# Optimization experiments

Measured on AMD Instinct MI355X. Metric: run time of the kernel, lower is better.

The kernel has to match this reference:

```python
import jax, jax.numpy as jnp
import numpy as np

B, H1, W1 = 2, 64, 64
H2, W2 = 64, 64
DIM = 64    # query_latent_dim
CLD = 128   # cost_latent_dim
K = 8       # latent tokens in cost memory
HEADS = 8
CH = 1      # cost_heads_num
R = 4


def layer_norm(x, g, b, eps=1e-5):
    m = x.mean(-1, keepdims=True)
    v = ((x - m) ** 2).mean(-1, keepdims=True)
    return (x - m) / jnp.sqrt(v + eps) * g + b


def lin_pos_emb(x, dim):
    # LinearPositionEmbeddingSine: x [N,1,2] -> [N,1,dim]
    freq = jnp.linspace(0.0, dim // 4 - 1, dim // 4)
    a = 3.14 * x[..., 0:1] * freq / 200.0
    b = 3.14 * x[..., 1:2] * freq / 200.0
    return jnp.concatenate([jnp.sin(a), jnp.cos(a), jnp.sin(b), jnp.cos(b)], axis=-1)


def bilinear_sample(img, coords):
    # img: [N,C,H,W]; coords: [N,h,w,2] (x,y) pixel coords; zero padding, align_corners=True
    N, C, H, W = img.shape
    x, y = coords[..., 0], coords[..., 1]
    x0 = jnp.floor(x); y0 = jnp.floor(y)
    wx = x - x0; wy = y - y0
    nidx = jnp.arange(N)[:, None, None]

    def gather(xi, yi):
        valid = ((xi >= 0) & (xi <= W - 1) & (yi >= 0) & (yi <= H - 1)).astype(img.dtype)
        xc = jnp.clip(xi, 0, W - 1).astype(jnp.int32)
        yc = jnp.clip(yi, 0, H - 1).astype(jnp.int32)
        return img[nidx, :, yc, xc] * valid[..., None]  # [N,h,w,C]

    v00 = gather(x0, y0); v10 = gather(x0 + 1.0, y0)
    v01 = gather(x0, y0 + 1.0); v11 = gather(x0 + 1.0, y0 + 1.0)
    out = (v00 * ((1 - wx) * (1 - wy))[..., None] + v10 * (wx * (1 - wy))[..., None]
           + v01 * ((1 - wx) * wy)[..., None] + v11 * (wx * wy)[..., None])
    return out.transpose(0, 3, 1, 2)  # [N,C,h,w]


def encode_flow(cost_maps, coords1):
    b, _, h1, w1 = coords1.shape
    c = coords1.transpose(0, 2, 3, 1)  # [B,H1,W1,2]
    d = jnp.linspace(-float(R), float(R), 2 * R + 1)
    dy, dx = jnp.meshgrid(d, d, indexing='ij')
    delta = jnp.stack([dy, dx], axis=-1)  # [9,9,2]
    centroid = c.reshape(b * h1 * w1, 1, 1, 2)
    samp = centroid + delta[None]  # [B*H1*W1,9,9,2]
    corr = bilinear_sample(cost_maps, samp)  # [B*H1*W1,CH,9,9]
    return corr.reshape(b, h1, w1, -1).transpose(0, 3, 1, 2)  # [B,81*CH,H1,W1]


def upsample_flow(flow, mask):
    # convex upsample [H,W] -> [8H,8W]
    n, _, h, w = flow.shape
    m = jax.nn.softmax(mask.reshape(n, 1, 9, 8, 8, h, w), axis=2)
    f = jnp.pad(8.0 * flow, ((0, 0), (0, 0), (1, 1), (1, 1)))
    patches = jnp.stack([f[:, :, i:i + h, j:j + w] for i in range(3) for j in range(3)], axis=2)
    up = jnp.sum(m * patches[:, :, :, None, None], axis=2)  # [N,2,8,8,H,W]
    return up.transpose(0, 1, 4, 2, 5, 3).reshape(n, 2, 8 * h, 8 * w)


def setup_inputs() -> dict:
    key = jax.random.key(0)
    ks = jax.random.split(key, 16)
    Bn = B * H1 * W1
    ys, xs = np.meshgrid(np.arange(H1), np.arange(W1), indexing='ij')
    grid = jnp.asarray(np.stack([xs, ys], 0), jnp.float32)  # [2,H1,W1], (x,y)
    coords1 = jnp.broadcast_to(grid, (B, 2, H1, W1)) + 3.0 * jax.random.normal(ks[0], (B, 2, H1, W1), jnp.float32)
    s = 0.05
    return {
        'cost_maps': jax.random.normal(ks[1], (Bn, CH, H2, W2), jnp.float32),
        'cost_memory': jax.random.normal(ks[2], (Bn, K, CLD), jnp.float32),
        'coords1': coords1,
        'up_mask': jax.random.normal(ks[3], (B, 9 * 64, H1, W1), jnp.float32),
        'fte_w1': s * jax.random.normal(ks[4], (DIM, 81 * CH), jnp.float32),
        'fte_b1': jnp.zeros((DIM,), jnp.float32),
        'fte_w2': s * jax.random.normal(ks[5], (DIM, DIM), jnp.float32),
        'fte_b2': jnp.zeros((DIM,), jnp.float32),
        'ln1_g': jnp.ones((DIM,), jnp.float32),
        'ln1_b': jnp.zeros((DIM,), jnp.float32),
        'ln2_g': jnp.ones((DIM,), jnp.float32),
        'ln2_b': jnp.zeros((DIM,), jnp.float32),
        'wq': s * jax.random.normal(ks[6], (DIM, DIM), jnp.float32),
        'bq': jnp.zeros((DIM,), jnp.float32),
        'wk': s * jax.random.normal(ks[7], (CLD, DIM), jnp.float32),
        'bk': jnp.zeros((DIM,), jnp.float32),
        'wv': s * jax.random.normal(ks[8], (CLD, DIM), jnp.float32),
        'bv': jnp.zeros((DIM,), jnp.float32),
        'wp': s * jax.random.normal(ks[9], (2 * DIM, DIM), jnp.float32),
        'bp': jnp.zeros((DIM,), jnp.float32),
        'ffn_w1': s * jax.random.normal(ks[10], (DIM, DIM), jnp.float32),
        'ffn_b1': jnp.zeros((DIM,), jnp.float32),
        'ffn_w2': s * jax.random.normal(ks[11], (DIM, DIM), jnp.float32),
        'ffn_b2': jnp.zeros((DIM,), jnp.float32),
    }


def reference(cost_maps, cost_memory, coords1, up_mask,
              fte_w1, fte_b1, fte_w2, fte_b2,
              ln1_g, ln1_b, ln2_g, ln2_b,
              wq, bq, wk, bk, wv, bv, wp, bp,
              ffn_w1, ffn_b1, ffn_w2, ffn_b2):
    Bn = B * H1 * W1
    ys, xs = jnp.meshgrid(jnp.arange(H1, dtype=coords1.dtype), jnp.arange(W1, dtype=coords1.dtype), indexing='ij')
    coords0 = jnp.broadcast_to(jnp.stack([xs, ys], 0), (B, 2, H1, W1))

    # correlation-volume bilinear sampling (encode_flow_token)
    corr = encode_flow(cost_maps, coords1)  # [B,81*CH,H1,W1]

    # flow token encoder: 1x1 conv -> GELU -> 1x1 conv
    q = jnp.einsum('bchw,oc->bohw', corr, fte_w1) + fte_b1[None, :, None, None]
    q = jax.nn.gelu(q, approximate=False)
    q = jnp.einsum('bchw,oc->bohw', q, fte_w2) + fte_b2[None, :, None, None]
    query = q.transpose(0, 2, 3, 1).reshape(Bn, 1, DIM)

    # cross attention with linear sine position encoding of query coords
    qc = coords1.reshape(B, 2, H1 * W1).transpose(0, 2, 1).reshape(Bn, 1, 2)
    enc = lin_pos_emb(qc, DIM)
    short = query
    qn = layer_norm(query, ln1_g, ln1_b)
    qlin = (qn + enc) @ wq + bq            # [Bn,1,DIM]
    k = cost_memory @ wk + bk              # [Bn,K,DIM]
    v = cost_memory @ wv + bv
    hd = DIM // HEADS
    qh = qlin.reshape(Bn, 1, HEADS, hd).transpose(0, 2, 1, 3)
    kh = k.reshape(Bn, K, HEADS, hd).transpose(0, 2, 1, 3)
    vh = v.reshape(Bn, K, HEADS, hd).transpose(0, 2, 1, 3)
    attn = jax.nn.softmax(jnp.einsum('bhid,bhjd->bhij', qh, kh) * (hd ** -0.5), axis=-1)
    out = jnp.einsum('bhij,bhjd->bhid', attn, vh).transpose(0, 2, 1, 3).reshape(Bn, 1, DIM)
    x = jnp.concatenate([out, short], -1) @ wp + bp
    x = short + x
    xn = layer_norm(x, ln2_g, ln2_b)
    x = x + (jax.nn.gelu(xn @ ffn_w1 + ffn_b1, approximate=False) @ ffn_w2 + ffn_b2)
    cost_global = x.reshape(B, H1, W1, DIM).transpose(0, 3, 1, 2)

    # convex upsampling of the flow field
    flow_up = upsample_flow(coords1 - coords0, up_mask)  # [B,2,8*H1,8*W1]
    return (flow_up, cost_global)
```

## Files before the change

kernel.cpp:

```cpp
#include <hip/hip_runtime.h>
#include <math.h>

typedef _Float16 h2 __attribute__((ext_vector_type(2)));

#if __has_builtin(__builtin_amdgcn_fdot2)
#define FDOT2(a,b,c) __builtin_amdgcn_fdot2((a),(b),(c),false)
#else
__device__ __forceinline__ float FDOT2(h2 a, h2 b, float c){
    return c + (float)a.x*(float)b.x + (float)a.y*(float)b.y;
}
#endif

__device__ __forceinline__ h2 pk2(float x, float y){
#if __has_builtin(__builtin_amdgcn_cvt_pkrtz)
    return __builtin_bit_cast(h2, __builtin_amdgcn_cvt_pkrtz(x, y));
#else
    h2 r; r.x = (_Float16)x; r.y = (_Float16)y; return r;
#endif
}
__device__ __forceinline__ unsigned h2u(h2 v){ return __builtin_bit_cast(unsigned, v); }
__device__ __forceinline__ h2 uh2(unsigned v){ return __builtin_bit_cast(h2, v); }

__device__ __forceinline__ float fast_rcp(float x){
#if __has_builtin(__builtin_amdgcn_rcpf)
    return __builtin_amdgcn_rcpf(x);
#else
    return 1.f/x;
#endif
}

__device__ __forceinline__ float dot8(uint4 w, uint4 v, float acc){
    acc = FDOT2(uh2(w.x), uh2(v.x), acc);
    acc = FDOT2(uh2(w.y), uh2(v.y), acc);
    acc = FDOT2(uh2(w.z), uh2(v.z), acc);
    acc = FDOT2(uh2(w.w), uh2(v.w), acc);
    return acc;
}

__device__ __forceinline__ float gelu_exact(float x){
    return 0.5f * x * (1.0f + erff(x * 0.70710678118654752f));
}

__device__ __forceinline__ void ln_stats(float x, float& mean, float& inv){
    float s1 = x, s2 = x*x;
    #pragma unroll
    for(int off = 32; off >= 1; off >>= 1){
        s1 += __shfl_xor(s1, off, 64);
        s2 += __shfl_xor(s2, off, 64);
    }
    mean = s1 * (1.f/64.f);
    float var = fmaxf(s2 * (1.f/64.f) - mean*mean, 0.f);
    inv = rsqrtf(var + 1e-5f);
}

__device__ __forceinline__ void lds_fence(){ __asm__ volatile("s_waitcnt lgkmcnt(0)" ::: "memory"); }

#define W1T_OFF 0
#define W2T_OFF 2816
#define WQ_OFF  5120
#define FW1_OFF 7424
#define FW2_OFF 9728
#define WV_OFF  12032
#define WP_OFF  16384
#define WK_OFF  20736
#define WTOT    25344

#define CMO   0
#define TUO   544
#define CORRO 544
#define QPO   1088
#define CCO   1124
#define PIXDW 1188
#define NWAVES 12
#define LDSDW (WTOT + NWAVES*PIXDW)

__global__ void prep_weights(const float* __restrict__ w1, const float* __restrict__ w2,
                             const float* __restrict__ wq, const float* __restrict__ fw1,
                             const float* __restrict__ fw2, const float* __restrict__ wv,
                             const float* __restrict__ wp, const float* __restrict__ wk,
                             unsigned* __restrict__ ws){
    int idx = blockIdx.x * blockDim.x + threadIdx.x;
    if(idx >= WTOT) return;
    float a = 0.f, b = 0.f;
    if(idx < W2T_OFF){
        int t = idx / 44, cp = idx % 44;
        if(2*cp   < 81) a = w1[t*81 + 2*cp];
        if(2*cp+1 < 81) b = w1[t*81 + 2*cp+1];
    } else if(idx < WQ_OFF){
        int r = idx - W2T_OFF; int t = r / 36, cp = r % 36;
        if(cp < 32){ a = w2[t*64 + 2*cp]; b = w2[t*64 + 2*cp+1]; }
    } else if(idx < FW1_OFF){
        int r = idx - WQ_OFF; int t = r / 36, cp = r % 36;
        if(cp < 32){ a = wq[(2*cp)*64 + t]; b = wq[(2*cp+1)*64 + t]; }
    } else if(idx < FW2_OFF){
        int r = idx - FW1_OFF; int t = r / 36, cp = r % 36;
        if(cp < 32){ a = fw1[(2*cp)*64 + t]; b = fw1[(2*cp+1)*64 + t]; }
    } else if(idx < WV_OFF){
        int r = idx - FW2_OFF; int t = r / 36, cp = r % 36;
        if(cp < 32){ a = fw2[(2*cp)*64 + t]; b = fw2[(2*cp+1)*64 + t]; }
    } else if(idx < WP_OFF){
        int r = idx - WV_OFF; int t = r / 68, cp = r % 68;
        if(cp < 64){ a = wv[(2*cp)*64 + t]; b = wv[(2*cp+1)*64 + t]; }
    } else if(idx < WK_OFF){
        int r = idx - WP_OFF; int t = r / 68, cp = r % 68;
        if(cp < 64){ a = wp[(2*cp)*64 + t]; b = wp[(2*cp+1)*64 + t]; }
    } else {
        int r = idx - WK_OFF; int c = r / 36, hp = r % 36;
        if(hp < 32){ a = wk[c*64 + 2*hp]; b = wk[c*64 + 2*hp+1]; }
    }
    ws[idx] = h2u(pk2(a, b));
}

__device__ __forceinline__ float bilin(const float* __restrict__ cmap, float cx, float cy, int e){
    int i = e / 9, j = e - 9*i;
    float sx = cx + (float)(i - 4);
    float sy = cy + (float)(j - 4);
    float x0 = floorf(sx), y0 = floorf(sy);
    float wx = sx - x0,   wy = sy - y0;
    float acc = 0.f;
    #pragma unroll
    for(int dy = 0; dy < 2; dy++){
        #pragma unroll
        for(int dx = 0; dx < 2; dx++){
            float xf = x0 + (float)dx, yf = y0 + (float)dy;
            bool valid = (xf >= 0.f) && (xf <= 63.f) && (yf >= 0.f) && (yf <= 63.f);
            int xi = min(max((int)xf, 0), 63);
            int yi = min(max((int)yf, 0), 63);
            float v = valid ? cmap[yi*64 + xi] : 0.f;
            acc += v * ((dx ? wx : 1.f - wx) * (dy ? wy : 1.f - wy));
        }
    }
    return acc;
}

__global__ __launch_bounds__(768, 1) void decoder_main(
    const float* __restrict__ cost_maps, const float* __restrict__ cost_memory,
    const float* __restrict__ coords1, const float* __restrict__ up_mask,
    const unsigned* __restrict__ ws,
    const float* __restrict__ fte_b1, const float* __restrict__ fte_b2,
    const float* __restrict__ ln1_g, const float* __restrict__ ln1_b,
    const float* __restrict__ ln2_g, const float* __restrict__ ln2_b,
    const float* __restrict__ bq, const float* __restrict__ bv,
    const float* __restrict__ bp, const float* __restrict__ fb1,
    const float* __restrict__ fb2, float* __restrict__ out)
{
    __shared__ unsigned sm[LDSDW];

    const int tid = threadIdx.x;
    const int wv  = tid >> 6;
    const int ln  = tid & 63;
    const int gw  = blockIdx.x * NWAVES + wv;
    const int nPix = (gw < 2048) ? 3 : 2;

    int pix = gw;
    const float4* cm4p = (const float4*)cost_memory;
    float4 cmv0 = cm4p[(size_t)pix*256 +   0 + ln];
    float4 cmv1 = cm4p[(size_t)pix*256 +  64 + ln];
    float4 cmv2 = cm4p[(size_t)pix*256 + 128 + ln];
    float4 cmv3 = cm4p[(size_t)pix*256 + 192 + ln];
    float cx = coords1[(pix >> 12)*8192 + (pix & 4095)];
    float cy = coords1[(pix >> 12)*8192 + 4096 + (pix & 4095)];

    {
        const uint4* src = (const uint4*)ws;
        uint4* dst = (uint4*)sm;
        for(int i = tid; i < WTOT/4; i += 768) dst[i] = src[i];
    }
    const float b1v = fte_b1[ln], b2v = fte_b2[ln];
    const float g1v = ln1_g[ln], be1 = ln1_b[ln];
    const float g2v = ln2_g[ln], be2 = ln2_b[ln];
    const float bqv = bq[ln], bvv = bv[ln], bpv = bp[ln];
    const float f1v = fb1[ln], f2v = fb2[ln];
    __syncthreads();

    float* out_cg = out + 2*2*512*512;
    unsigned* P = sm + WTOT + wv * PIXDW;

    const int h_ = ln & 7;
    const int c0 = ln >> 3;
    const int j_ = ln >> 3;
    const int h3 = ln >> 3;

    #pragma unroll 1
    for(int g = 0; g < nPix; g++){
        {
            float4 v; int l0, jt, cp0;
            #define STAGE(V, I4) \
                v = V; l0 = 4*((I4)*64 + ln); jt = l0 >> 7; cp0 = (l0 & 127) >> 1; \
                { uint2 pw; pw.x = h2u(pk2(v.x, v.y)); pw.y = h2u(pk2(v.z, v.w)); \
                  *(uint2*)&P[CMO + jt*68 + cp0] = pw; }
            STAGE(cmv0, 0) STAGE(cmv1, 1) STAGE(cmv2, 2) STAGE(cmv3, 3)
            #undef STAGE
        }
        {
            const float* cmap = cost_maps + (size_t)pix * 4096;
            float cv = bilin(cmap, cx, cy, ln);
            float c2 = bilin(cmap, cx, cy, 64 + ln);
            float pr = __shfl_xor(cv, 1, 64);
            if((ln & 1) == 0) P[CORRO + (ln >> 1)] = h2u(pk2(cv, pr));
            float pr2 = __shfl_xor(c2, 1, 64);
            if(ln < 17 && (ln & 1) == 0){
                float bb = (ln == 16) ? 0.f : pr2;
                P[CORRO + 32 + (ln >> 1)] = h2u(pk2(c2, bb));
            }
            if(ln < 3) P[CORRO + 41 + ln] = 0u;
        }
        int npix = pix + 3072;
        float4 n0, n1, n2, n3; float ncx = 0.f, ncy = 0.f;
        if(g + 1 < nPix){
            n0 = cm4p[(size_t)npix*256 +   0 + ln];
            n1 = cm4p[(size_t)npix*256 +  64 + ln];
            n2 = cm4p[(size_t)npix*256 + 128 + ln];
            n3 = cm4p[(size_t)npix*256 + 192 + ln];
            ncx = coords1[(npix >> 12)*8192 + (npix & 4095)];
            ncy = coords1[(npix >> 12)*8192 + 4096 + (npix & 4095)];
        }
        lds_fence();

        float q1;
        {
            const uint4* wr = (const uint4*)&sm[W1T_OFF + ln*44];
            const uint4* ar = (const uint4*)&P[CORRO];
            float a0 = b1v, a1 = 0.f;
            #pragma unroll
            for(int gg = 0; gg < 10; gg += 2){
                a0 = dot8(wr[gg],   ar[gg],   a0);
                a1 = dot8(wr[gg+1], ar[gg+1], a1);
            }
            a0 = dot8(wr[10], ar[10], a0);
            q1 = a0 + a1;
        }
        q1 = gelu_exact(q1);
        {
            float pr = __shfl_xor(q1, 1, 64);
            if((ln & 1) == 0) P[QPO + (ln >> 1)] = h2u(pk2(q1, pr));
        }
        lds_fence();
        float shortv;
        {
            const uint4* wr = (const uint4*)&sm[W2T_OFF + ln*36];
            const uint4* ar = (const uint4*)&P[QPO];
            float a0 = b2v, a1 = 0.f;
            #pragma unroll
            for(int gg = 0; gg < 8; gg += 2){
                a0 = dot8(wr[gg],   ar[gg],   a0);
                a1 = dot8(wr[gg+1], ar[gg+1], a1);
            }
            shortv = a0 + a1;
        }
        {
            float psv = __shfl_xor(shortv, 1, 64);
            if((ln & 1) == 0) P[CCO + 32 + (ln >> 1)] = h2u(pk2(shortv, psv));
        }
        float mean, inv1;
        ln_stats(shortv, mean, inv1);
        float qn = (shortv - mean) * inv1 * g1v + be1;
        {
            int   fi    = ln & 15;
            float coord = (ln < 32) ? cx : cy;
            float ang   = 3.14f * coord * (float)fi / 200.0f;
            float enc   = (ln & 16) ? __cosf(ang) : __sinf(ang);
            float qv    = qn + enc;
            float pr = __shfl_xor(qv, 1, 64);
            if((ln & 1) == 0) P[QPO + (ln >> 1)] = h2u(pk2(qv, pr));
        }
        lds_fence();
        float qlin;
        {
            const uint4* wr = (const uint4*)&sm[WQ_OFF + ln*36];
            const uint4* ar = (const uint4*)&P[QPO];
            float a0 = bqv, a1 = 0.f;
            #pragma unroll
            for(int gg = 0; gg < 8; gg += 2){
                a0 = dot8(wr[gg],   ar[gg],   a0);
                a1 = dot8(wr[gg+1], ar[gg+1], a1);
            }
            qlin = a0 + a1;
        }
        {
            uint4 qh4;
            {
                float v0 = __shfl(qlin, h_*8 + 0, 64), v1 = __shfl(qlin, h_*8 + 1, 64);
                float v2 = __shfl(qlin, h_*8 + 2, 64), v3 = __shfl(qlin, h_*8 + 3, 64);
                float v4 = __shfl(qlin, h_*8 + 4, 64), v5 = __shfl(qlin, h_*8 + 5, 64);
                float v6 = __shfl(qlin, h_*8 + 6, 64), v7 = __shfl(qlin, h_*8 + 7, 64);
                qh4.x = h2u(pk2(v0, v1)); qh4.y = h2u(pk2(v2, v3));
                qh4.z = h2u(pk2(v4, v5)); qh4.w = h2u(pk2(v6, v7));
            }
            #pragma unroll
            for(int i = 0; i < 16; i++){
                int c = c0 + 8*i;
                uint4 wk4 = *(const uint4*)&sm[WK_OFF + c*36 + h_*4];
                float tv = dot8(wk4, qh4, 0.f);
                float prt = __shfl_xor(tv, 8, 64);
                if((c0 & 1) == 0) P[TUO + h_*68 + (c0 >> 1) + 4*i] = h2u(pk2(tv, prt));
            }
        }
        lds_fence();
        float sacc;
        {
            const int hk = ln & 7;
            const uint4* cmr = (const uint4*)&P[CMO + j_*68];
            const uint4* tur = (const uint4*)&P[TUO + hk*68];
            float s0 = 0.f, s1 = 0.f, s2 = 0.f, s3 = 0.f;
            #pragma unroll
            for(int gg = 0; gg < 16; gg += 4){
                s0 = dot8(cmr[gg],   tur[gg],   s0);
                s1 = dot8(cmr[gg+1], tur[gg+1], s1);
                s2 = dot8(cmr[gg+2], tur[gg+2], s2);
                s3 = dot8(cmr[gg+3], tur[gg+3], s3);
            }
            sacc = (s0 + s1) + (s2 + s3);
        }
        float p;
        {
            float sc = sacc * 0.35355339059327373f;
            float mx = sc;
            mx = fmaxf(mx, __shfl_xor(mx,  8, 64));
            mx = fmaxf(mx, __shfl_xor(mx, 16, 64));
            mx = fmaxf(mx, __shfl_xor(mx, 32, 64));
            float ex = __expf(sc - mx);
            float se = ex;
            se += __shfl_xor(se,  8, 64);
            se += __shfl_xor(se, 16, 64);
            se += __shfl_xor(se, 32, 64);
            p = ex * fast_rcp(se);
        }
        {
            float av[8];
            #pragma unroll
            for(int j = 0; j < 8; j++) av[j] = __shfl(p, j*8 + h_, 64);
            h2 u0 = pk2(0.f,0.f), u1 = u0, u2 = u0, u3 = u0;
            h2 u4 = u0, u5 = u0, u6 = u0, u7 = u0;
            #pragma unroll
            for(int j = 0; j < 8; j++){
                h2 aj = pk2(av[j], av[j]);
                const uint4* cmr = (const uint4*)&P[CMO + j*68 + 8*c0];
                uint4 qa = cmr[0], qb = cmr[1];
                u0 += aj * uh2(qa.x); u1 += aj * uh2(qa.y);
                u2 += aj * uh2(qa.z); u3 += aj * uh2(qa.w);
                u4 += aj * uh2(qb.x); u5 += aj * uh2(qb.y);
                u6 += aj * uh2(qb.z); u7 += aj * uh2(qb.w);
            }
            uint4 wa; wa.x = h2u(u0); wa.y = h2u(u1); wa.z = h2u(u2); wa.w = h2u(u3);
            uint4 wb; wb.x = h2u(u4); wb.y = h2u(u5); wb.z = h2u(u6); wb.w = h2u(u7);
            *(uint4*)&P[TUO + h_*68 + 8*c0]     = wa;
            *(uint4*)&P[TUO + h_*68 + 8*c0 + 4] = wb;
        }
        lds_fence();
        float attno;
        {
            const uint4* ur = (const uint4*)&P[TUO + h3*68];
            const uint4* wr = (const uint4*)&sm[WV_OFF + ln*68];
            float a0 = bvv, a1 = 0.f, a2 = 0.f, a3 = 0.f;
            #pragma unroll
            for(int gg = 0; gg < 16; gg += 4){
                a0 = dot8(ur[gg],   wr[gg],   a0);
                a1 = dot8(ur[gg+1], wr[gg+1], a1);
                a2 = dot8(ur[gg+2], wr[gg+2], a2);
                a3 = dot8(ur[gg+3], wr[gg+3], a3);
            }
            attno = (a0 + a1) + (a2 + a3);
        }
        {
            float pa = __shfl_xor(attno, 1, 64);
            if((ln & 1) == 0) P[CCO + (ln >> 1)] = h2u(pk2(attno, pa));
        }
        lds_fence();
        float x;
        {
            const uint4* wr = (const uint4*)&sm[WP_OFF + ln*68];
            const uint4* ar = (const uint4*)&P[CCO];
            float a0 = bpv, a1 = 0.f, a2 = 0.f, a3 = 0.f;
            #pragma unroll
            for(int gg = 0; gg < 16; gg += 4){
                a0 = dot8(wr[gg],   ar[gg],   a0);
                a1 = dot8(wr[gg+1], ar[gg+1], a1);
                a2 = dot8(wr[gg+2], ar[gg+2], a2);
                a3 = dot8(wr[gg+3], ar[gg+3], a3);
            }
            x = (a0 + a1) + (a2 + a3);
        }
        x += shortv;
        float m2, inv2;
        ln_stats(x, m2, inv2);
        float xn = (x - m2) * inv2 * g2v + be2;
        {
            float pr = __shfl_xor(xn, 1, 64);
            if((ln & 1) == 0) P[QPO + (ln >> 1)] = h2u(pk2(xn, pr));
        }
        lds_fence();
        float h1v;
        {
            const uint4* wr = (const uint4*)&sm[FW1_OFF + ln*36];
            const uint4* ar = (const uint4*)&P[QPO];
            float a0 = f1v, a1 = 0.f;
            #pragma unroll
            for(int gg = 0; gg < 8; gg += 2){
                a0 = dot8(wr[gg],   ar[gg],   a0);
                a1 = dot8(wr[gg+1], ar[gg+1], a1);
            }
            h1v = a0 + a1;
        }
        h1v = gelu_exact(h1v);
        {
            float pr = __shfl_xor(h1v, 1, 64);
            if((ln & 1) == 0) P[QPO + (ln >> 1)] = h2u(pk2(h1v, pr));
        }
        lds_fence();
        float f2;
        {
            const uint4* wr = (const uint4*)&sm[FW2_OFF + ln*36];
            const uint4* ar = (const uint4*)&P[QPO];
            float a0 = f2v, a1 = 0.f;
            #pragma unroll
            for(int gg = 0; gg < 8; gg += 2){
                a0 = dot8(wr[gg],   ar[gg],   a0);
                a1 = dot8(wr[gg+1], ar[gg+1], a1);
            }
            f2 = a0 + a1;
        }
        x += f2;
        {
            int bb = pix >> 12, hh = (pix >> 6) & 63, ww = pix & 63;
            out_cg[(((size_t)(bb*64 + ln))*64 + hh)*64 + ww] = x;
        }
        pix = npix; cx = ncx; cy = ncy;
        cmv0 = n0; cmv1 = n1; cmv2 = n2; cmv3 = n3;
    }

    if(gw >= 2048){
        const int u  = gw - 2048;
        const int ub = u >> 9, uh = (u >> 3) & 63, ur = u & 7;
        const int w  = ln;

        float fx[3], fy[3];
        #pragma unroll
        for(int i = 0; i < 3; i++){
            int hh = uh + i - 1;
            bool ok = (hh >= 0) && (hh < 64);
            int hc = min(max(hh, 0), 63);
            float cxv = coords1[((ub*2 + 0)*64 + hc)*64 + w];
            float cyv = coords1[((ub*2 + 1)*64 + hc)*64 + w];
            fx[i] = ok ? 8.f * (cxv - (float)w)  : 0.f;
            fy[i] = ok ? 8.f * (cyv - (float)hh) : 0.f;
        }
        float fxm[3], fxp[3], fym[3], fyp[3];
        #pragma unroll
        for(int i = 0; i < 3; i++){
            fxm[i] = __shfl(fx[i], w - 1, 64);
            fxp[i] = __shfl(fx[i], w + 1, 64);
            fym[i] = __shfl(fy[i], w - 1, 64);
            fyp[i] = __shfl(fy[i], w + 1, 64);
            if(w == 0) { fxm[i] = 0.f; fym[i] = 0.f; }
            if(w == 63){ fxp[i] = 0.f; fyp[i] = 0.f; }
        }
        #pragma unroll
        for(int sh = 0; sh < 8; sh += 4){
            float m[36];
            #pragma unroll
            for(int k = 0; k < 9; k++){
                #pragma unroll
                for(int si = 0; si < 4; si++){
                    int c = k*64 + ur*8 + sh + si;
                    m[k*4 + si] = up_mask[(((size_t)ub*576 + c)*64 + uh)*64 + w];
                }
            }
            float outx[4], outy[4];
            #pragma unroll
            for(int si = 0; si < 4; si++){
                float mx = m[si];
                #pragma unroll
                for(int k = 1; k < 9; k++) mx = fmaxf(mx, m[k*4 + si]);
                float e, se = 0.f, ox = 0.f, oy = 0.f;
                #pragma unroll
                for(int k = 0; k < 9; k++){
                    e = __expf(m[k*4 + si] - mx);
                    se += e;
                    int i = k / 3, j = k % 3;
                    float fxv = (j == 0) ? fxm[i] : ((j == 1) ? fx[i] : fxp[i]);
                    float fyv = (j == 0) ? fym[i] : ((j == 1) ? fy[i] : fyp[i]);
                    ox += e * fxv;
                    oy += e * fyv;
                }
                float inv = fast_rcp(se);
                outx[si] = ox * inv;
                outy[si] = oy * inv;
            }
            size_t row = (size_t)(uh*8 + ur) * 512 + w*8 + sh;
            *(float4*)&out[(size_t)(ub*2 + 0)*262144 + row] = *(const float4*)outx;
            *(float4*)&out[(size_t)(ub*2 + 1)*262144 + row] = *(const float4*)outy;
        }
    }
}

extern "C" void kernel_launch(void* const* d_in, const int* in_sizes, int n_in,
                              void* d_out, int out_size, void* d_ws, size_t ws_size,
                              hipStream_t stream)
{
    const float* cost_maps   = (const float*)d_in[0];
    const float* cost_memory = (const float*)d_in[1];
    const float* coords1     = (const float*)d_in[2];
    const float* up_mask     = (const float*)d_in[3];
    const float* fte_w1      = (const float*)d_in[4];
    const float* fte_b1      = (const float*)d_in[5];
    const float* fte_w2      = (const float*)d_in[6];
    const float* fte_b2      = (const float*)d_in[7];
    const float* ln1_g       = (const float*)d_in[8];
    const float* ln1_b       = (const float*)d_in[9];
    const float* ln2_g       = (const float*)d_in[10];
    const float* ln2_b       = (const float*)d_in[11];
    const float* wq          = (const float*)d_in[12];
    const float* bq          = (const float*)d_in[13];
    const float* wk          = (const float*)d_in[14];
    const float* bv          = (const float*)d_in[17];
    const float* wv          = (const float*)d_in[16];
    const float* wp          = (const float*)d_in[18];
    const float* bp          = (const float*)d_in[19];
    const float* fw1         = (const float*)d_in[20];
    const float* fb1         = (const float*)d_in[21];
    const float* fw2         = (const float*)d_in[22];
    const float* fb2         = (const float*)d_in[23];
    float* out = (float*)d_out;
    unsigned* wsu = (unsigned*)d_ws;

    prep_weights<<<(WTOT + 511)/512, 512, 0, stream>>>(
        fte_w1, fte_w2, wq, fw1, fw2, wv, wp, wk, wsu);

    decoder_main<<<256, 768, 0, stream>>>(
        cost_maps, cost_memory, coords1, up_mask, wsu,
        fte_b1, fte_b2, ln1_g, ln1_b, ln2_g, ln2_b,
        bq, bv, bp, fb1, fb2,
        out);
}
```

Baseline: 259.0 us.

## Widen blocks to 14 waves, shrink per-wave LDS, defer softmax normalization

Raises each block from 12 to 14 waves by overlapping the per-wave LDS regions (query, concat and transposed buffers now alias the cost-memory staging area). The pixel and upsample work is redistributed so that every block does the same share of both. The attention softmax is left unnormalized until after the value projection, where one reciprocal multiply per output replaces the per-probability divide. The upsample loop now handles one sub-pixel at a time with scalar stores to lower register pressure. The aliased LDS regions could create hazards, and the scalar stores are less coalesced.

```diff
diff --git a/kernel.cpp b/kernel.cpp
--- a/kernel.cpp
+++ b/kernel.cpp
@@ -68,10 +68,10 @@
 #define CMO   0
 #define TUO   544
 #define CORRO 544
-#define QPO   1088
-#define CCO   1124
-#define PIXDW 1188
-#define NWAVES 12
+#define QPO   544
+#define CCO   0
+#define PIXDW 1088
+#define NWAVES 14
 #define LDSDW (WTOT + NWAVES*PIXDW)
 
 __global__ void prep_weights(const float* __restrict__ w1, const float* __restrict__ w2,
@@ -133,7 +133,7 @@
     return acc;
 }
 
-__global__ __launch_bounds__(768, 1) void decoder_main(
+__global__ __launch_bounds__(896, 4) void decoder_main(
     const float* __restrict__ cost_maps, const float* __restrict__ cost_memory,
     const float* __restrict__ coords1, const float* __restrict__ up_mask,
     const unsigned* __restrict__ ws,
@@ -150,7 +150,8 @@
     const int wv  = tid >> 6;
     const int ln  = tid & 63;
     const int gw  = blockIdx.x * NWAVES + wv;
-    const int nPix = (gw < 2048) ? 3 : 2;
+    const int nPix = (wv < 4) ? 3 : 2;
+    const int p2 = 7168 + blockIdx.x * 4 + wv;
 
     int pix = gw;
     const float4* cm4p = (const float4*)cost_memory;
@@ -164,7 +165,7 @@
     {
         const uint4* src = (const uint4*)ws;
         uint4* dst = (uint4*)sm;
-        for(int i = tid; i < WTOT/4; i += 768) dst[i] = src[i];
+        for(int i = tid; i < WTOT/4; i += 896) dst[i] = src[i];
     }
     const float b1v = fte_b1[ln], b2v = fte_b2[ln];
     const float g1v = ln1_g[ln], be1 = ln1_b[ln];
@@ -205,7 +206,7 @@
             }
             if(ln < 3) P[CORRO + 41 + ln] = 0u;
         }
-        int npix = pix + 3072;
+        int npix = (g == 0) ? pix + 3584 : p2;
         float4 n0, n1, n2, n3; float ncx = 0.f, ncy = 0.f;
         if(g + 1 < nPix){
             n0 = cm4p[(size_t)npix*256 +   0 + ln];
@@ -248,10 +249,6 @@
             }
             shortv = a0 + a1;
         }
-        {
-            float psv = __shfl_xor(shortv, 1, 64);
-            if((ln & 1) == 0) P[CCO + 32 + (ln >> 1)] = h2u(pk2(shortv, psv));
-        }
         float mean, inv1;
         ln_stats(shortv, mean, inv1);
         float qn = (shortv - mean) * inv1 * g1v + be1;
@@ -312,24 +309,26 @@
             }
             sacc = (s0 + s1) + (s2 + s3);
         }
-        float p;
+        float ex, invse;
         {
             float sc = sacc * 0.35355339059327373f;
             float mx = sc;
             mx = fmaxf(mx, __shfl_xor(mx,  8, 64));
             mx = fmaxf(mx, __shfl_xor(mx, 16, 64));
             mx = fmaxf(mx, __shfl_xor(mx, 32, 64));
-            float ex = __expf(sc - mx);
-            float se = ex;
-            se += __shfl_xor(se,  8, 64);
-            se += __shfl_xor(se, 16, 64);
-            se += __shfl_xor(se, 32, 64);
-            p = ex * fast_rcp(se);
+            ex = __expf(sc - mx);
         }
         {
             float av[8];
             #pragma unroll
-            for(int j = 0; j < 8; j++) av[j] = __shfl(p, j*8 + h_, 64);
+            for(int j = 0; j < 8; j++) av[j] = __shfl(ex, j*8 + h_, 64);
+            {
+                float se = ex;
+                se += __shfl_xor(se,  8, 64);
+                se += __shfl_xor(se, 16, 64);
+                se += __shfl_xor(se, 32, 64);
+                invse = fast_rcp(se);
+            }
             h2 u0 = pk2(0.f,0.f), u1 = u0, u2 = u0, u3 = u0;
             h2 u4 = u0, u5 = u0, u6 = u0, u7 = u0;
             #pragma unroll
@@ -350,9 +349,10 @@
         lds_fence();
         float attno;
         {
+            float invh = __shfl(invse, h3, 64);
             const uint4* ur = (const uint4*)&P[TUO + h3*68];
             const uint4* wr = (const uint4*)&sm[WV_OFF + ln*68];
-            float a0 = bvv, a1 = 0.f, a2 = 0.f, a3 = 0.f;
+            float a0 = 0.f, a1 = 0.f, a2 = 0.f, a3 = 0.f;
             #pragma unroll
             for(int gg = 0; gg < 16; gg += 4){
                 a0 = dot8(ur[gg],   wr[gg],   a0);
@@ -360,11 +360,13 @@
                 a2 = dot8(ur[gg+2], wr[gg+2], a2);
                 a3 = dot8(ur[gg+3], wr[gg+3], a3);
             }
-            attno = (a0 + a1) + (a2 + a3);
+            attno = fmaf((a0 + a1) + (a2 + a3), invh, bvv);
         }
         {
             float pa = __shfl_xor(attno, 1, 64);
             if((ln & 1) == 0) P[CCO + (ln >> 1)] = h2u(pk2(attno, pa));
+            float psv = __shfl_xor(shortv, 1, 64);
+            if((ln & 1) == 0) P[CCO + 32 + (ln >> 1)] = h2u(pk2(shortv, psv));
         }
         lds_fence();
         float x;
@@ -429,8 +431,8 @@
         cmv0 = n0; cmv1 = n1; cmv2 = n2; cmv3 = n3;
     }
 
-    if(gw >= 2048){
-        const int u  = gw - 2048;
+    if(wv >= 4 && wv < 8){
+        const int u  = blockIdx.x * 4 + (wv - 4);
         const int ub = u >> 9, uh = (u >> 3) & 63, ur = u & 7;
         const int w  = ln;
 
@@ -455,41 +457,34 @@
             if(w == 0) { fxm[i] = 0.f; fym[i] = 0.f; }
             if(w == 63){ fxp[i] = 0.f; fyp[i] = 0.f; }
         }
-        #pragma unroll
-        for(int sh = 0; sh < 8; sh += 4){
-            float m[36];
+        const size_t row = (size_t)(uh*8 + ur) * 512 + (size_t)w*8;
+        float* outx_p = out + (size_t)(ub*2 + 0)*262144 + row;
+        float* outy_p = out + (size_t)(ub*2 + 1)*262144 + row;
+        #pragma unroll 2
+        for(int s8 = 0; s8 < 8; s8++){
+            float m[9];
             #pragma unroll
             for(int k = 0; k < 9; k++){
-                #pragma unroll
-                for(int si = 0; si < 4; si++){
-                    int c = k*64 + ur*8 + sh + si;
-                    m[k*4 + si] = up_mask[(((size_t)ub*576 + c)*64 + uh)*64 + w];
-                }
-            }
-            float outx[4], outy[4];
-            #pragma unroll
-            for(int si = 0; si < 4; si++){
-                float mx = m[si];
-                #pragma unroll
-                for(int k = 1; k < 9; k++) mx = fmaxf(mx, m[k*4 + si]);
-                float e, se = 0.f, ox = 0.f, oy = 0.f;
-                #pragma unroll
-                for(int k = 0; k < 9; k++){
-                    e = __expf(m[k*4 + si] - mx);
-                    se += e;
-                    int i = k / 3, j = k % 3;
-                    float fxv = (j == 0) ? fxm[i] : ((j == 1) ? fx[i] : fxp[i]);
-                    float fyv = (j == 0) ? fym[i] : ((j == 1) ? fy[i] : fyp[i]);
-                    ox += e * fxv;
-                    oy += e * fyv;
-                }
-                float inv = fast_rcp(se);
-                outx[si] = ox * inv;
-                outy[si] = oy * inv;
-            }
-            size_t row = (size_t)(uh*8 + ur) * 512 + w*8 + sh;
-            *(float4*)&out[(size_t)(ub*2 + 0)*262144 + row] = *(const float4*)outx;
-            *(float4*)&out[(size_t)(ub*2 + 1)*262144 + row] = *(const float4*)outy;
+                int c = k*64 + ur*8 + s8;
+                m[k] = up_mask[(((size_t)ub*576 + c)*64 + uh)*64 + w];
+            }
+            float mx = m[0];
+            #pragma unroll
+            for(int k = 1; k < 9; k++) mx = fmaxf(mx, m[k]);
+            float se = 0.f, ox = 0.f, oy = 0.f;
+            #pragma unroll
+            for(int k = 0; k < 9; k++){
+                float e = __expf(m[k] - mx);
+                se += e;
+                int i = k / 3, j = k % 3;
+                float fxv = (j == 0) ? fxm[i] : ((j == 1) ? fx[i] : fxp[i]);
+                float fyv = (j == 0) ? fym[i] : ((j == 1) ? fy[i] : fyp[i]);
+                ox += e * fxv;
+                oy += e * fyv;
+            }
+            float inv = fast_rcp(se);
+            outx_p[s8] = ox * inv;
+            outy_p[s8] = oy * inv;
         }
     }
 }
@@ -527,7 +522,7 @@
     prep_weights<<<(WTOT + 511)/512, 512, 0, stream>>>(
         fte_w1, fte_w2, wq, fw1, fw2, wv, wp, wk, wsu);
 
-    decoder_main<<<256, 768, 0, stream>>>(
+    decoder_main<<<256, 896, 0, stream>>>(
         cost_maps, cost_memory, coords1, up_mask, wsu,
         fte_b1, fte_b2, ln1_g, ln1_b, ln2_g, ln2_b,
         bq, bv, bp, fb1, fb2,
```

Result: no change. 259.1 us (+0.0%).
